# Optimization experiments

Measured on AMD Instinct MI355X. Metric: run time of the kernel, lower is better.

## Reference

```python
import jax, jax.numpy as jnp
import numpy as np

TOP_K = 2
Z_LOSS_COEFF = 1e-5


def setup_inputs() -> dict:
    key = jax.random.key(0)
    ks = jax.random.split(key, 6)
    B, S, D, H, E = 2, 2048, 768, 2688, 8  # hidden = int(3.5 * dim)
    scale = 0.02
    return {
        "x": jax.random.normal(ks[0], (B, S, D), dtype=jnp.float32),
        "gate_w": (jax.random.normal(ks[1], (E, D), dtype=jnp.float32) * scale),  # router Linear [out=E, in=D]
        "expert_bias": jnp.zeros((E,), dtype=jnp.float32),  # load-balancing bias buffer (zeros at init)
        "w_gate": (jax.random.normal(ks[2], (E, D, H), dtype=jnp.float32) * scale),
        "w_up": (jax.random.normal(ks[3], (E, D, H), dtype=jnp.float32) * scale),
        "w_down": (jax.random.normal(ks[4], (E, H, D), dtype=jnp.float32) * scale),
    }


def reference(x, gate_w, expert_bias, w_gate, w_up, w_down):
    B, S, D = x.shape
    E = gate_w.shape[0]

    # ---- Router ----
    logits = jnp.einsum('bsd,ed->bse', x, gate_w)                 # [B,S,E]
    sel_logits_biased = logits + expert_bias                      # bias only affects selection
    _, idx = jax.lax.top_k(sel_logits_biased, TOP_K)              # [B,S,K] int32
    selected_logits = jnp.take_along_axis(logits, idx, axis=-1)  # weights from UNbiased logits
    weights = jax.nn.softmax(selected_logits, axis=-1)            # [B,S,K]
    z_loss = Z_LOSS_COEFF * jnp.mean(jax.nn.logsumexp(logits, axis=-1) ** 2)

    # ---- Combine weights: [B,S,E], zero for unselected experts ----
    combine = jnp.sum(jax.nn.one_hot(idx, E, dtype=x.dtype) * weights[..., None], axis=2)

    # ---- Expert SwiGLU MLPs (grouped GEMM over all experts; masked-combine) ----
    xf = x.reshape(-1, D)            # [T,D]
    cf = combine.reshape(-1, E)      # [T,E]
    g = jax.nn.silu(jnp.einsum('td,edh->teh', xf, w_gate))        # [T,E,H]
    u = jnp.einsum('td,edh->teh', xf, w_up)                       # [T,E,H]
    y = jnp.einsum('teh,ehd->ted', g * u, w_down)                 # [T,E,D]
    out = jnp.einsum('ted,te->td', y, cf).reshape(B, S, D)
    return out, z_loss
```

## Files before the change

### kernel.cpp

```cpp
#include <hip/hip_runtime.h>
#include <hip/hip_bf16.h>
#include <math.h>

typedef __bf16 bf16;
typedef bf16 bf16x2 __attribute__((ext_vector_type(2)));
typedef bf16 bf16x4 __attribute__((ext_vector_type(4)));
typedef bf16 bf16x8 __attribute__((ext_vector_type(8)));
typedef float f32x4 __attribute__((ext_vector_type(4)));

#define T_TOK 4096
#define DDIM  768
#define HDIM  2688
#define NEXP  8
#define RMAX  9216
#define NMT   (RMAX / 128)
#define NT1   (HDIM / 64)
#define NT2   (DDIM / 128)
#define KHALF (HDIM / 2)
#define NK1   (DDIM / 64)
#define NK2   (KHALF / 64)
#define RBLK  (T_TOK / 4)

__device__ __forceinline__ void async_copy16(const void* g, void* l) {
    __builtin_amdgcn_global_load_lds(
        (__attribute__((address_space(1))) void*)g,
        (__attribute__((address_space(3))) void*)l,
        16, 0, 0);
}

#define LGKM0 do { asm volatile("s_waitcnt lgkmcnt(0)" ::: "memory"); __builtin_amdgcn_sched_barrier(0); } while(0)
#define VMC4  asm volatile("s_waitcnt vmcnt(4)" ::: "memory")
#define VMC0  asm volatile("s_waitcnt vmcnt(0)" ::: "memory")
#define BAR   __builtin_amdgcn_s_barrier()

__global__ void router_kernel(const float* __restrict__ x,
                              const float* __restrict__ gate_w,
                              const float* __restrict__ ebias,
                              int* __restrict__ tok_e,
                              float* __restrict__ tok_w,
                              int* __restrict__ cpart,
                              float* __restrict__ zpart) {
    __shared__ float gw[NEXP * DDIM];
    __shared__ int hist[NEXP];
    __shared__ float z4[4];
    int tid = threadIdx.x;
    if (tid < NEXP) hist[tid] = 0;
    for (int i = tid; i < NEXP * DDIM / 4; i += 256)
        ((float4*)gw)[i] = ((const float4*)gate_w)[i];
    __syncthreads();

    int wv = tid >> 6, lane = tid & 63;
    int t = blockIdx.x * 4 + wv;
    const float* xr = x + (size_t)t * DDIM;

    float4 xv[3];
#pragma unroll
    for (int j = 0; j < 3; ++j) xv[j] = ((const float4*)xr)[j * 64 + lane];

    float acc[NEXP];
#pragma unroll
    for (int e = 0; e < NEXP; ++e) {
        float a = 0.f;
#pragma unroll
        for (int j = 0; j < 3; ++j) {
            float4 w = ((const float4*)(gw + e * DDIM))[j * 64 + lane];
            a += xv[j].x * w.x + xv[j].y * w.y + xv[j].z * w.z + xv[j].w * w.w;
        }
        acc[e] = a;
    }
#pragma unroll
    for (int e = 0; e < NEXP; ++e) {
#pragma unroll
        for (int off = 32; off > 0; off >>= 1) acc[e] += __shfl_xor(acc[e], off);
    }

    if (lane == 0) {
        float b[NEXP];
#pragma unroll
        for (int e = 0; e < NEXP; ++e) b[e] = acc[e] + ebias[e];
        int i0 = 0;
#pragma unroll
        for (int e = 1; e < NEXP; ++e) if (b[e] > b[i0]) i0 = e;
        int i1 = (i0 == 0) ? 1 : 0;
        float b1 = b[i1];
#pragma unroll
        for (int e = 0; e < NEXP; ++e) if (e != i0 && b[e] > b1) { b1 = b[e]; i1 = e; }

        float l0 = acc[i0], l1 = acc[i1];
        float mx = fmaxf(l0, l1);
        float e0 = __expf(l0 - mx), e1 = __expf(l1 - mx);
        float inv = 1.f / (e0 + e1);
        tok_e[t * 2 + 0] = i0;
        tok_e[t * 2 + 1] = i1;
        tok_w[t * 2 + 0] = e0 * inv;
        tok_w[t * 2 + 1] = e1 * inv;
        atomicAdd(&hist[i0], 1);
        atomicAdd(&hist[i1], 1);

        float m8 = acc[0];
#pragma unroll
        for (int e = 1; e < NEXP; ++e) m8 = fmaxf(m8, acc[e]);
        float s = 0.f;
#pragma unroll
        for (int e = 0; e < NEXP; ++e) s += __expf(acc[e] - m8);
        float lse = m8 + __logf(s);
        z4[wv] = lse * lse;
    }
    __syncthreads();
    if (tid < NEXP) cpart[blockIdx.x * NEXP + tid] = hist[tid];
    if (tid == NEXP) zpart[blockIdx.x] = z4[0] + z4[1] + z4[2] + z4[3];
}

__global__ void setup_kernel(int* __restrict__ ctrl,
                             const int* __restrict__ cpart,
                             const float* __restrict__ zpart,
                             const int* __restrict__ tok_e,
                             int* __restrict__ pair_tok,
                             int* __restrict__ tok_pos,
                             float* __restrict__ zloss) {
    __shared__ int whist[16][NEXP];
    __shared__ float wz[16];
    __shared__ int scnt[NEXP];
    int tid = threadIdx.x;
    int wv = tid >> 6, lane = tid & 63;

    int h[NEXP];
#pragma unroll
    for (int e = 0; e < NEXP; ++e) h[e] = cpart[tid * NEXP + e];
    float z = zpart[tid];
#pragma unroll
    for (int off = 32; off > 0; off >>= 1) {
#pragma unroll
        for (int e = 0; e < NEXP; ++e) h[e] += __shfl_xor(h[e], off);
        z += __shfl_xor(z, off);
    }
    if (lane == 0) {
#pragma unroll
        for (int e = 0; e < NEXP; ++e) whist[wv][e] = h[e];
        wz[wv] = z;
    }
    __syncthreads();
    if (tid == 0) {
        float zs = 0.f;
        for (int w = 0; w < 16; ++w) zs += wz[w];
        *zloss = (1e-5f / (float)T_TOK) * zs;
        int off = 0;
        for (int e = 0; e < NEXP; ++e) {
            int c = 0;
            for (int w = 0; w < 16; ++w) c += whist[w][e];
            ctrl[e] = c;
            ctrl[16 + e] = off;
            scnt[e] = off;
            off += (c + 127) & ~127;
        }
        ctrl[16 + NEXP] = off;
    }
    __syncthreads();
    for (int t = tid; t < T_TOK; t += 1024) {
#pragma unroll
        for (int k = 0; k < 2; ++k) {
            int e = tok_e[t * 2 + k];
            int pos = atomicAdd(&scnt[e], 1);
            pair_tok[pos] = t;
            tok_pos[t * 2 + k] = pos;
        }
    }
}

__global__ void gather_kernel(const float* __restrict__ x,
                              const int* __restrict__ ctrl,
                              const int* __restrict__ pair_tok,
                              bf16* __restrict__ Xg) {
    int r = blockIdx.x;
    int tid = threadIdx.x;
    const int* offs = ctrl + 16;
    int total = offs[8];
    int tok = -1;
    if (r < total) {
        int e = 0;
#pragma unroll
        for (int i = 1; i < NEXP; ++i) if (r >= offs[i]) e = i;
        if (r - offs[e] < ctrl[e]) tok = pair_tok[r];
    }
    bf16x4 o;
    if (tok >= 0) {
        float4 v = *(const float4*)(x + (size_t)tok * DDIM + tid * 4);
        o.x = (bf16)v.x; o.y = (bf16)v.y; o.z = (bf16)v.z; o.w = (bf16)v.w;
    } else {
        o.x = (bf16)0.f; o.y = (bf16)0.f; o.z = (bf16)0.f; o.w = (bf16)0.f;
    }
    *(bf16x4*)(Xg + (size_t)r * DDIM + tid * 4) = o;
}

__global__ void transpose_kernel(const float* __restrict__ wgp,
                                 const float* __restrict__ wup,
                                 const float* __restrict__ wdp,
                                 bf16* __restrict__ WgT,
                                 bf16* __restrict__ WuT,
                                 bf16* __restrict__ WdT) {
    __shared__ float tile[64 * 64];
    int m = blockIdx.y;
    int kind = m >> 3, e = m & 7;
    const float* src; bf16* dst; int R, C;
    if (kind == 0)      { src = wgp + (size_t)e * DDIM * HDIM; dst = WgT + (size_t)e * HDIM * DDIM; R = DDIM; C = HDIM; }
    else if (kind == 1) { src = wup + (size_t)e * DDIM * HDIM; dst = WuT + (size_t)e * HDIM * DDIM; R = DDIM; C = HDIM; }
    else                { src = wdp + (size_t)e * HDIM * DDIM; dst = WdT + (size_t)e * DDIM * HDIM; R = HDIM; C = DDIM; }

    int nR = R >> 6;
    int t = blockIdx.x;
    int tr = t % nR, tc = t / nR;
    int r0 = tr << 6, c0 = tc << 6;
    int tid = threadIdx.x;

#pragma unroll
    for (int i = 0; i < 4; ++i) {
        int idx = i * 256 + tid;
        int rr = idx >> 4, c4 = idx & 15;
        int cs = c4 ^ ((rr >> 3) & 3);
        float4 v = *(const float4*)(src + (size_t)(r0 + rr) * C + c0 + c4 * 4);
        *(float4*)&tile[rr * 64 + cs * 4] = v;
    }
    __syncthreads();

#pragma unroll
    for (int i = 0; i < 2; ++i) {
        int idx = i * 256 + tid;
        int cc = idx >> 3, rp0 = (idx & 7) * 8;
        bf16x8 o;
#pragma unroll
        for (int j = 0; j < 8; ++j) {
            int r = rp0 + j;
            o[j] = (bf16)tile[r * 64 + (((cc >> 2) ^ ((r >> 3) & 3)) << 2) + (cc & 3)];
        }
        *(bf16x8*)(dst + (size_t)(c0 + cc) * R + r0 + rp0) = o;
    }
}

__launch_bounds__(256)
__global__ void gemm1_kernel(const bf16* __restrict__ Xg,
                             const bf16* __restrict__ WgT,
                             const bf16* __restrict__ WuT,
                             const int* __restrict__ ctrl,
                             bf16* __restrict__ G) {
    extern __shared__ __align__(16) bf16 smem[];

    int bid = blockIdx.x;
    int id = (bid & 7) * (NMT * NT1 / 8) + (bid >> 3);
    int gm = id / NT1, nt = id % NT1;
    const int* offs = ctrl + 16;
    int row0 = gm * 128;
    if (row0 >= offs[NEXP]) return;
    int e = 0;
#pragma unroll
    for (int i = 1; i < NEXP; ++i) if (row0 >= offs[i]) e = i;
    int n0 = nt * 64;

    int tid = threadIdx.x;
    int wv = tid >> 6, lane = tid & 63;
    int wm = wv & 1, wn = wv >> 1;
    int quad = lane >> 4, lm = lane & 15;

    const bf16* srcA[4];
    const bf16* srcB[4];
#pragma unroll
    for (int j = 0; j < 4; ++j) {
        int c = j * 256 + tid;
        int r = c >> 3, q = c & 7;
        srcA[j] = Xg + (size_t)(row0 + r) * DDIM + (q ^ (r & 7)) * 8;
        const bf16* wb = (j < 2) ? (WgT + ((size_t)e * HDIM + n0 + r) * DDIM)
                                 : (WuT + ((size_t)e * HDIM + n0 + (r - 64)) * DDIM);
        srcB[j] = wb + (q ^ (r & 7)) * 8;
    }

#define STG_A1(KT, BUF) do { int ko_ = (KT) * 64; \
    _Pragma("unroll") for (int j_ = 0; j_ < 4; ++j_) \
        async_copy16(srcA[j_] + ko_, smem + (BUF) * 8192 + (j_ * 256 + tid) * 8); } while (0)
#define STG_B1(KT, BUF) do { int ko_ = (KT) * 64; \
    _Pragma("unroll") for (int j_ = 0; j_ < 4; ++j_) \
        async_copy16(srcB[j_] + ko_, smem + 16384 + (BUF) * 8192 + (j_ * 256 + tid) * 8); } while (0)

    int aOff = (wm * 64 + lm) * 64;
    int bOff = (wn * 32 + lm) * 64;
    int cA = (quad ^ (lm & 7)) * 8;

    f32x4 accg[4][2], accu[4][2];
#pragma unroll
    for (int mi = 0; mi < 4; ++mi)
#pragma unroll
        for (int nf = 0; nf < 2; ++nf) { accg[mi][nf] = 0.f; accu[mi][nf] = 0.f; }

    STG_A1(0, 0);
    STG_B1(0, 0);

#pragma unroll
    for (int kt = 0; kt < NK1; ++kt) {
        const int buf = kt & 1;
        const bf16* pa = smem + buf * 8192;
        const bf16* pb = smem + 16384 + buf * 8192;
        if (kt + 1 < NK1) { STG_A1(kt + 1, buf ^ 1); VMC4; }
        else              { VMC0; }
        BAR;

        bf16x8 af[4][2], bbg[2][2], bbu[2][2];
#pragma unroll
        for (int mi = 0; mi < 4; ++mi)
#pragma unroll
            for (int ks = 0; ks < 2; ++ks)
                af[mi][ks] = *(const bf16x8*)(pa + aOff + mi * 1024 + (cA ^ (ks * 32)));
#pragma unroll
        for (int nf = 0; nf < 2; ++nf)
#pragma unroll
            for (int ks = 0; ks < 2; ++ks)
                bbg[nf][ks] = *(const bf16x8*)(pb + bOff + nf * 1024 + (cA ^ (ks * 32)));
        LGKM0;
        __builtin_amdgcn_s_setprio(1);
#pragma unroll
        for (int mi = 0; mi < 4; ++mi)
#pragma unroll
            for (int nf = 0; nf < 2; ++nf)
#pragma unroll
                for (int ks = 0; ks < 2; ++ks)
                    accg[mi][nf] = __builtin_amdgcn_mfma_f32_16x16x32_bf16(af[mi][ks], bbg[nf][ks], accg[mi][nf], 0, 0, 0);
        __builtin_amdgcn_s_setprio(0);

        if (kt + 1 < NK1) STG_B1(kt + 1, buf ^ 1);

#pragma unroll
        for (int nf = 0; nf < 2; ++nf)
#pragma unroll
            for (int ks = 0; ks < 2; ++ks)
                bbu[nf][ks] = *(const bf16x8*)(pb + 4096 + bOff + nf * 1024 + (cA ^ (ks * 32)));
        LGKM0;
        __builtin_amdgcn_s_setprio(1);
#pragma unroll
        for (int mi = 0; mi < 4; ++mi)
#pragma unroll
            for (int nf = 0; nf < 2; ++nf)
#pragma unroll
                for (int ks = 0; ks < 2; ++ks)
                    accu[mi][nf] = __builtin_amdgcn_mfma_f32_16x16x32_bf16(af[mi][ks], bbu[nf][ks], accu[mi][nf], 0, 0, 0);
        __builtin_amdgcn_s_setprio(0);
        BAR;
    }

#pragma unroll
    for (int mi = 0; mi < 4; ++mi)
#pragma unroll
        for (int nj = 0; nj < 2; ++nj)
#pragma unroll
            for (int r = 0; r < 4; ++r) {
                float gg = accg[mi][nj][r];
                float u = accu[mi][nj][r];
                float val = (gg / (1.f + __expf(-gg))) * u;
                int rl = wm * 64 + mi * 16 + quad * 4 + r;
                int c  = wn * 32 + nj * 16 + lm;
                smem[rl * 72 + c] = (bf16)val;
            }
    __syncthreads();
#pragma unroll
    for (int i = 0; i < 4; ++i) {
        int idx = (i * 256 + tid) * 8;
        int row = idx >> 6, c = idx & 63;
        bf16x8 v = *(const bf16x8*)(smem + row * 72 + c);
        *(bf16x8*)(G + (size_t)(row0 + row) * HDIM + n0 + c) = v;
    }
#undef STG_A1
#undef STG_B1
}

__launch_bounds__(256)
__global__ void gemm2_kernel(const bf16* __restrict__ G,
                             const bf16* __restrict__ WdT,
                             const int* __restrict__ ctrl,
                             bf16* __restrict__ Ya,
                             bf16* __restrict__ Yb) {
    extern __shared__ __align__(16) bf16 smem[];

    int bid = blockIdx.x;
    int id = (bid & 7) * (NMT * NT2 * 2 / 8) + (bid >> 3);
    int gm = id / (NT2 * 2);
    int r2 = id % (NT2 * 2);
    int nt = r2 >> 1, s = r2 & 1;
    const int* offs = ctrl + 16;
    int row0 = gm * 128;
    if (row0 >= offs[NEXP]) return;
    int e = 0;
#pragma unroll
    for (int i = 1; i < NEXP; ++i) if (row0 >= offs[i]) e = i;
    int n0 = nt * 128;

    int tid = threadIdx.x;
    int wv = tid >> 6, lane = tid & 63;
    int wm = wv & 1, wn = wv >> 1;
    int quad = lane >> 4, lm = lane & 15;

    const bf16* srcA[4];
    const bf16* srcB[4];
#pragma unroll
    for (int j = 0; j < 4; ++j) {
        int c = j * 256 + tid;
        int r = c >> 3, q = c & 7;
        srcA[j] = G + (size_t)(row0 + r) * HDIM + s * KHALF + (q ^ (r & 7)) * 8;
        srcB[j] = WdT + ((size_t)e * DDIM + n0 + r) * HDIM + s * KHALF + (q ^ (r & 7)) * 8;
    }

#define STG_A2(KT, BUF) do { int ko_ = (KT) * 64; \
    _Pragma("unroll") for (int j_ = 0; j_ < 4; ++j_) \
        async_copy16(srcA[j_] + ko_, smem + (BUF) * 8192 + (j_ * 256 + tid) * 8); } while (0)
#define STG_B2(KT, BUF) do { int ko_ = (KT) * 64; \
    _Pragma("unroll") for (int j_ = 0; j_ < 4; ++j_) \
        async_copy16(srcB[j_] + ko_, smem + 16384 + (BUF) * 8192 + (j_ * 256 + tid) * 8); } while (0)

    int aOff = (wm * 64 + lm) * 64;
    int bOff = (wn * 64 + lm) * 64;
    int cA = (quad ^ (lm & 7)) * 8;

    f32x4 acc[4][4];
#pragma unroll
    for (int mi = 0; mi < 4; ++mi)
#pragma unroll
        for (int nf = 0; nf < 4; ++nf) acc[mi][nf] = 0.f;

    STG_A2(0, 0);
    STG_B2(0, 0);

#pragma unroll
    for (int kt = 0; kt < NK2; ++kt) {
        const int buf = kt & 1;
        const bf16* pa = smem + buf * 8192;
        const bf16* pb = smem + 16384 + buf * 8192;
        if (kt + 1 < NK2) { STG_A2(kt + 1, buf ^ 1); VMC4; }
        else              { VMC0; }
        BAR;

        bf16x8 af[4][2], bb[4][2];
#pragma unroll
        for (int mi = 0; mi < 4; ++mi)
#pragma unroll
            for (int ks = 0; ks < 2; ++ks)
                af[mi][ks] = *(const bf16x8*)(pa + aOff + mi * 1024 + (cA ^ (ks * 32)));
#pragma unroll
        for (int nf = 0; nf < 2; ++nf)
#pragma unroll
            for (int ks = 0; ks < 2; ++ks)
                bb[nf][ks] = *(const bf16x8*)(pb + bOff + nf * 1024 + (cA ^ (ks * 32)));
        LGKM0;
        __builtin_amdgcn_s_setprio(1);
#pragma unroll
        for (int mi = 0; mi < 4; ++mi)
#pragma unroll
            for (int nf = 0; nf < 2; ++nf)
#pragma unroll
                for (int ks = 0; ks < 2; ++ks)
                    acc[mi][nf] = __builtin_amdgcn_mfma_f32_16x16x32_bf16(af[mi][ks], bb[nf][ks], acc[mi][nf], 0, 0, 0);
        __builtin_amdgcn_s_setprio(0);

        if (kt + 1 < NK2) STG_B2(kt + 1, buf ^ 1);

#pragma unroll
        for (int nf = 2; nf < 4; ++nf)
#pragma unroll
            for (int ks = 0; ks < 2; ++ks)
                bb[nf][ks] = *(const bf16x8*)(pb + bOff + nf * 1024 + (cA ^ (ks * 32)));
        LGKM0;
        __builtin_amdgcn_s_setprio(1);
#pragma unroll
        for (int mi = 0; mi < 4; ++mi)
#pragma unroll
            for (int nf = 2; nf < 4; ++nf)
#pragma unroll
                for (int ks = 0; ks < 2; ++ks)
                    acc[mi][nf] = __builtin_amdgcn_mfma_f32_16x16x32_bf16(af[mi][ks], bb[nf][ks], acc[mi][nf], 0, 0, 0);
        __builtin_amdgcn_s_setprio(0);
        BAR;
    }

    bf16* Y = s ? Yb : Ya;
#pragma unroll
    for (int rr = 0; rr < 2; ++rr) {
#pragma unroll
        for (int mi = 0; mi < 4; ++mi)
#pragma unroll
            for (int nj = 0; nj < 2; ++nj) {
                int ni = rr * 2 + nj;
#pragma unroll
                for (int r = 0; r < 4; ++r) {
                    int rl = wm * 64 + mi * 16 + quad * 4 + r;
                    int c  = wn * 32 + nj * 16 + lm;
                    smem[rl * 72 + c] = (bf16)acc[mi][ni][r];
                }
            }
        __syncthreads();
#pragma unroll
        for (int i = 0; i < 4; ++i) {
            int idx = (i * 256 + tid) * 8;
            int row = idx >> 6, c = idx & 63;
            bf16x8 v = *(const bf16x8*)(smem + row * 72 + c);
            int col = n0 + ((c >> 5) << 6) + (c & 31) + rr * 32;
            *(bf16x8*)(Y + (size_t)(row0 + row) * DDIM + col) = v;
        }
        if (rr == 0) __syncthreads();
    }
#undef STG_A2
#undef STG_B2
}

__global__ void combine_kernel(const bf16* __restrict__ Ya,
                               const bf16* __restrict__ Yb,
                               const int* __restrict__ tok_pos,
                               const float* __restrict__ tok_w,
                               float* __restrict__ out) {
    int t = blockIdx.x;
    int i = threadIdx.x;
    int p0 = tok_pos[t * 2 + 0], p1 = tok_pos[t * 2 + 1];
    float w0 = tok_w[t * 2 + 0], w1 = tok_w[t * 2 + 1];
    bf16x4 a0 = *(const bf16x4*)(Ya + (size_t)p0 * DDIM + i * 4);
    bf16x4 b0 = *(const bf16x4*)(Yb + (size_t)p0 * DDIM + i * 4);
    bf16x4 a1 = *(const bf16x4*)(Ya + (size_t)p1 * DDIM + i * 4);
    bf16x4 b1 = *(const bf16x4*)(Yb + (size_t)p1 * DDIM + i * 4);
    float4 o;
    o.x = w0 * ((float)a0.x + (float)b0.x) + w1 * ((float)a1.x + (float)b1.x);
    o.y = w0 * ((float)a0.y + (float)b0.y) + w1 * ((float)a1.y + (float)b1.y);
    o.z = w0 * ((float)a0.z + (float)b0.z) + w1 * ((float)a1.z + (float)b1.z);
    o.w = w0 * ((float)a0.w + (float)b0.w) + w1 * ((float)a1.w + (float)b1.w);
    *(float4*)(out + (size_t)t * DDIM + i * 4) = o;
}

extern "C" void kernel_launch(void* const* d_in, const int* in_sizes, int n_in,
                              void* d_out, int out_size, void* d_ws, size_t ws_size,
                              hipStream_t stream) {
    const float* x      = (const float*)d_in[0];
    const float* gate_w = (const float*)d_in[1];
    const float* ebias  = (const float*)d_in[2];
    const float* wgp    = (const float*)d_in[3];
    const float* wup    = (const float*)d_in[4];
    const float* wdp    = (const float*)d_in[5];
    float* out = (float*)d_out;

    int*   ctrl     = (int*)d_ws;
    int*   tok_e    = ctrl + 128;
    float* tok_w    = (float*)(tok_e + 2 * T_TOK);
    int*   pair_tok = (int*)(tok_w + 2 * T_TOK);
    int*   tok_pos  = pair_tok + RMAX;
    int*   cpart    = tok_pos + 2 * T_TOK;
    float* zpart    = (float*)(cpart + RBLK * NEXP);
    bf16*  Xg       = (bf16*)(zpart + RBLK);
    bf16*  Ya       = Xg;
    bf16*  Yb       = Xg + (size_t)RMAX * DDIM;
    bf16*  G        = Yb + (size_t)RMAX * DDIM;
    bf16*  WgT      = G + (size_t)RMAX * HDIM;
    bf16*  WuT      = WgT + (size_t)NEXP * DDIM * HDIM;
    bf16*  WdT      = WuT + (size_t)NEXP * DDIM * HDIM;

    hipMemsetAsync(out + (size_t)T_TOK * DDIM, 0, sizeof(float), stream);
    hipMemsetAsync(d_ws, 0, 512, stream);

    router_kernel<<<RBLK, 256, 0, stream>>>(x, gate_w, ebias, tok_e, tok_w, cpart, zpart);
    setup_kernel<<<1, 1024, 0, stream>>>(ctrl, cpart, zpart, tok_e, pair_tok, tok_pos,
                                         out + (size_t)T_TOK * DDIM);
    transpose_kernel<<<dim3(504, 24), 256, 0, stream>>>(wgp, wup, wdp, WgT, WuT, WdT);
    gather_kernel<<<RMAX, 192, 0, stream>>>(x, ctrl, pair_tok, Xg);
    gemm1_kernel<<<NMT * NT1, 256, 65536, stream>>>(Xg, WgT, WuT, ctrl, G);
    gemm2_kernel<<<NMT * NT2 * 2, 256, 65536, stream>>>(G, WdT, ctrl, Ya, Yb);
    combine_kernel<<<T_TOK, 192, 0, stream>>>(Ya, Yb, tok_pos, tok_w, out);
}
```

Baseline: 384.0 us.

## Merge router and weight transpose into one launch; issue B prefetch earlier

After: 371.8 us. 3.2% less time.

```diff
diff --git a/kernel.cpp b/kernel.cpp
--- a/kernel.cpp
+++ b/kernel.cpp
@@ -20,6 +20,7 @@
 #define NK1   (DDIM / 64)
 #define NK2   (KHALF / 64)
 #define RBLK  (T_TOK / 4)
+#define TBLK  12096
 
 __device__ __forceinline__ void async_copy16(const void* g, void* l) {
     __builtin_amdgcn_global_load_lds(
@@ -29,28 +30,76 @@
 }
 
 #define LGKM0 do { asm volatile("s_waitcnt lgkmcnt(0)" ::: "memory"); __builtin_amdgcn_sched_barrier(0); } while(0)
-#define VMC4  asm volatile("s_waitcnt vmcnt(4)" ::: "memory")
+#define VMC8  asm volatile("s_waitcnt vmcnt(8)" ::: "memory")
 #define VMC0  asm volatile("s_waitcnt vmcnt(0)" ::: "memory")
 #define BAR   __builtin_amdgcn_s_barrier()
 
-__global__ void router_kernel(const float* __restrict__ x,
-                              const float* __restrict__ gate_w,
-                              const float* __restrict__ ebias,
-                              int* __restrict__ tok_e,
-                              float* __restrict__ tok_w,
-                              int* __restrict__ cpart,
-                              float* __restrict__ zpart) {
-    __shared__ float gw[NEXP * DDIM];
+__global__ void prep_kernel(const float* __restrict__ wgp,
+                            const float* __restrict__ wup,
+                            const float* __restrict__ wdp,
+                            bf16* __restrict__ WgT,
+                            bf16* __restrict__ WuT,
+                            bf16* __restrict__ WdT,
+                            const float* __restrict__ x,
+                            const float* __restrict__ gate_w,
+                            const float* __restrict__ ebias,
+                            int* __restrict__ tok_e,
+                            float* __restrict__ tok_w,
+                            int* __restrict__ cpart,
+                            float* __restrict__ zpart) {
+    __shared__ __align__(16) float shbuf[NEXP * DDIM];
     __shared__ int hist[NEXP];
     __shared__ float z4[4];
+    int b = blockIdx.x;
     int tid = threadIdx.x;
+
+    if (b < TBLK) {
+        float* tile = shbuf;
+        int m = b / 504, t = b % 504;
+        int kind = m >> 3, e = m & 7;
+        const float* src; bf16* dst; int R, C;
+        if (kind == 0)      { src = wgp + (size_t)e * DDIM * HDIM; dst = WgT + (size_t)e * HDIM * DDIM; R = DDIM; C = HDIM; }
+        else if (kind == 1) { src = wup + (size_t)e * DDIM * HDIM; dst = WuT + (size_t)e * HDIM * DDIM; R = DDIM; C = HDIM; }
+        else                { src = wdp + (size_t)e * HDIM * DDIM; dst = WdT + (size_t)e * DDIM * HDIM; R = HDIM; C = DDIM; }
+
+        int nR = R >> 6;
+        int tr = t % nR, tc = t / nR;
+        int r0 = tr << 6, c0 = tc << 6;
+
+#pragma unroll
+        for (int i = 0; i < 4; ++i) {
+            int idx = i * 256 + tid;
+            int rr = idx >> 4, c4 = idx & 15;
+            int cs = c4 ^ ((rr >> 3) & 3);
+            float4 v = *(const float4*)(src + (size_t)(r0 + rr) * C + c0 + c4 * 4);
+            *(float4*)&tile[rr * 64 + cs * 4] = v;
+        }
+        __syncthreads();
+
+#pragma unroll
+        for (int i = 0; i < 2; ++i) {
+            int idx = i * 256 + tid;
+            int cc = idx >> 3, rp0 = (idx & 7) * 8;
+            bf16x8 o;
+#pragma unroll
+            for (int j = 0; j < 8; ++j) {
+                int r = rp0 + j;
+                o[j] = (bf16)tile[r * 64 + (((cc >> 2) ^ ((r >> 3) & 3)) << 2) + (cc & 3)];
+            }
+            *(bf16x8*)(dst + (size_t)(c0 + cc) * R + r0 + rp0) = o;
+        }
+        return;
+    }
+
+    int rb = b - TBLK;
+    float* gw = shbuf;
     if (tid < NEXP) hist[tid] = 0;
     for (int i = tid; i < NEXP * DDIM / 4; i += 256)
         ((float4*)gw)[i] = ((const float4*)gate_w)[i];
     __syncthreads();
 
     int wv = tid >> 6, lane = tid & 63;
-    int t = blockIdx.x * 4 + wv;
+    int t = rb * 4 + wv;
     const float* xr = x + (size_t)t * DDIM;
 
     float4 xv[3];
@@ -75,16 +124,16 @@
     }
 
     if (lane == 0) {
-        float b[NEXP];
-#pragma unroll
-        for (int e = 0; e < NEXP; ++e) b[e] = acc[e] + ebias[e];
+        float bb[NEXP];
+#pragma unroll
+        for (int e = 0; e < NEXP; ++e) bb[e] = acc[e] + ebias[e];
         int i0 = 0;
 #pragma unroll
-        for (int e = 1; e < NEXP; ++e) if (b[e] > b[i0]) i0 = e;
+        for (int e = 1; e < NEXP; ++e) if (bb[e] > bb[i0]) i0 = e;
         int i1 = (i0 == 0) ? 1 : 0;
-        float b1 = b[i1];
-#pragma unroll
-        for (int e = 0; e < NEXP; ++e) if (e != i0 && b[e] > b1) { b1 = b[e]; i1 = e; }
+        float b1 = bb[i1];
+#pragma unroll
+        for (int e = 0; e < NEXP; ++e) if (e != i0 && bb[e] > b1) { b1 = bb[e]; i1 = e; }
 
         float l0 = acc[i0], l1 = acc[i1];
         float mx = fmaxf(l0, l1);
@@ -107,8 +156,8 @@
         z4[wv] = lse * lse;
     }
     __syncthreads();
-    if (tid < NEXP) cpart[blockIdx.x * NEXP + tid] = hist[tid];
-    if (tid == NEXP) zpart[blockIdx.x] = z4[0] + z4[1] + z4[2] + z4[3];
+    if (tid < NEXP) cpart[rb * NEXP + tid] = hist[tid];
+    if (tid == NEXP) zpart[rb] = z4[0] + z4[1] + z4[2] + z4[3];
 }
 
 __global__ void setup_kernel(int* __restrict__ ctrl,
@@ -192,50 +241,6 @@
     *(bf16x4*)(Xg + (size_t)r * DDIM + tid * 4) = o;
 }
 
-__global__ void transpose_kernel(const float* __restrict__ wgp,
-                                 const float* __restrict__ wup,
-                                 const float* __restrict__ wdp,
-                                 bf16* __restrict__ WgT,
-                                 bf16* __restrict__ WuT,
-                                 bf16* __restrict__ WdT) {
-    __shared__ float tile[64 * 64];
-    int m = blockIdx.y;
-    int kind = m >> 3, e = m & 7;
-    const float* src; bf16* dst; int R, C;
-    if (kind == 0)      { src = wgp + (size_t)e * DDIM * HDIM; dst = WgT + (size_t)e * HDIM * DDIM; R = DDIM; C = HDIM; }
-    else if (kind == 1) { src = wup + (size_t)e * DDIM * HDIM; dst = WuT + (size_t)e * HDIM * DDIM; R = DDIM; C = HDIM; }
-    else                { src = wdp + (size_t)e * HDIM * DDIM; dst = WdT + (size_t)e * DDIM * HDIM; R = HDIM; C = DDIM; }
-
-    int nR = R >> 6;
-    int t = blockIdx.x;
-    int tr = t % nR, tc = t / nR;
-    int r0 = tr << 6, c0 = tc << 6;
-    int tid = threadIdx.x;
-
-#pragma unroll
-    for (int i = 0; i < 4; ++i) {
-        int idx = i * 256 + tid;
-        int rr = idx >> 4, c4 = idx & 15;
-        int cs = c4 ^ ((rr >> 3) & 3);
-        float4 v = *(const float4*)(src + (size_t)(r0 + rr) * C + c0 + c4 * 4);
-        *(float4*)&tile[rr * 64 + cs * 4] = v;
-    }
-    __syncthreads();
-
-#pragma unroll
-    for (int i = 0; i < 2; ++i) {
-        int idx = i * 256 + tid;
-        int cc = idx >> 3, rp0 = (idx & 7) * 8;
-        bf16x8 o;
-#pragma unroll
-        for (int j = 0; j < 8; ++j) {
-            int r = rp0 + j;
-            o[j] = (bf16)tile[r * 64 + (((cc >> 2) ^ ((r >> 3) & 3)) << 2) + (cc & 3)];
-        }
-        *(bf16x8*)(dst + (size_t)(c0 + cc) * R + r0 + rp0) = o;
-    }
-}
-
 __launch_bounds__(256)
 __global__ void gemm1_kernel(const bf16* __restrict__ Xg,
                              const bf16* __restrict__ WgT,
@@ -297,7 +302,7 @@
         const int buf = kt & 1;
         const bf16* pa = smem + buf * 8192;
         const bf16* pb = smem + 16384 + buf * 8192;
-        if (kt + 1 < NK1) { STG_A1(kt + 1, buf ^ 1); VMC4; }
+        if (kt + 1 < NK1) { STG_A1(kt + 1, buf ^ 1); STG_B1(kt + 1, buf ^ 1); VMC8; }
         else              { VMC0; }
         BAR;
 
@@ -322,8 +327,6 @@
                 for (int ks = 0; ks < 2; ++ks)
                     accg[mi][nf] = __builtin_amdgcn_mfma_f32_16x16x32_bf16(af[mi][ks], bbg[nf][ks], accg[mi][nf], 0, 0, 0);
         __builtin_amdgcn_s_setprio(0);
-
-        if (kt + 1 < NK1) STG_B1(kt + 1, buf ^ 1);
 
 #pragma unroll
         for (int nf = 0; nf < 2; ++nf)
@@ -429,7 +432,7 @@
         const int buf = kt & 1;
         const bf16* pa = smem + buf * 8192;
         const bf16* pb = smem + 16384 + buf * 8192;
-        if (kt + 1 < NK2) { STG_A2(kt + 1, buf ^ 1); VMC4; }
+        if (kt + 1 < NK2) { STG_A2(kt + 1, buf ^ 1); STG_B2(kt + 1, buf ^ 1); VMC8; }
         else              { VMC0; }
         BAR;
 
@@ -454,8 +457,6 @@
                 for (int ks = 0; ks < 2; ++ks)
                     acc[mi][nf] = __builtin_amdgcn_mfma_f32_16x16x32_bf16(af[mi][ks], bb[nf][ks], acc[mi][nf], 0, 0, 0);
         __builtin_amdgcn_s_setprio(0);
-
-        if (kt + 1 < NK2) STG_B2(kt + 1, buf ^ 1);
 
 #pragma unroll
         for (int nf = 2; nf < 4; ++nf)
@@ -555,10 +556,10 @@
     hipMemsetAsync(out + (size_t)T_TOK * DDIM, 0, sizeof(float), stream);
     hipMemsetAsync(d_ws, 0, 512, stream);
 
-    router_kernel<<<RBLK, 256, 0, stream>>>(x, gate_w, ebias, tok_e, tok_w, cpart, zpart);
+    prep_kernel<<<TBLK + RBLK, 256, 0, stream>>>(wgp, wup, wdp, WgT, WuT, WdT,
+                                                 x, gate_w, ebias, tok_e, tok_w, cpart, zpart);
     setup_kernel<<<1, 1024, 0, stream>>>(ctrl, cpart, zpart, tok_e, pair_tok, tok_pos,
                                          out + (size_t)T_TOK * DDIM);
-    transpose_kernel<<<dim3(504, 24), 256, 0, stream>>>(wgp, wup, wdp, WgT, WuT, WdT);
     gather_kernel<<<RMAX, 192, 0, stream>>>(x, ctrl, pair_tok, Xg);
     gemm1_kernel<<<NMT * NT1, 256, 65536, stream>>>(Xg, WgT, WuT, ctrl, G);
     gemm2_kernel<<<NMT * NT2 * 2, 256, 65536, stream>>>(G, WdT, ctrl, Ya, Yb);
```
